# Optimization experiments

Measured on AMD Instinct MI355X. Metric: run time of the kernel, lower is better.

## Reference

```python
import jax, jax.numpy as jnp
import numpy as np

B = 8388608  # ~4096 stocks x 2048 trading days
D = 2048     # unique dates
LAMBDA_VOL = 0.85
LAMBDA_DIR = 0.15
TEMPERATURE = 5.0
EPS = 1e-6


def setup_inputs() -> dict:
    key = jax.random.key(0)
    k1, k2, k3, k4, k5 = jax.random.split(key, 5)
    return {
        "direction_logits": jax.random.normal(k1, (B, 2), dtype=jnp.float32),
        "direction_labels": jax.random.randint(k2, (B,), 0, 2, dtype=jnp.int64),
        "volatility_pred": jax.random.uniform(k3, (B,), dtype=jnp.float32),
        "volatility_target": jax.random.uniform(k4, (B,), dtype=jnp.float32),
        "dates": jax.random.randint(k5, (B,), 0, D, dtype=jnp.int64),
        "num_dates": D,
    }


def reference(direction_logits, direction_labels, volatility_pred, volatility_target, dates, num_dates):
    # ---- QLIKE volatility loss (masked mean) ----
    tgt, pred = volatility_target, volatility_pred
    vol_valid = (~jnp.isnan(tgt)) & (tgt > EPS) & (pred > EPS)
    pred_var = jnp.maximum(pred * pred, EPS)
    true_var = jnp.maximum(tgt * tgt, EPS)
    qlike = true_var / pred_var + jnp.log(pred_var)
    n_valid = jnp.sum(vol_valid)
    vol_loss = jnp.where(
        n_valid > 0,
        jnp.sum(jnp.where(vol_valid, qlike, 0.0)) / jnp.maximum(n_valid, 1).astype(qlike.dtype),
        0.0,
    )

    # ---- ListNet ranking loss via segmented softmax over dates ----
    dvalid = direction_labels >= 0
    p1 = jax.nn.softmax(direction_logits, axis=1)[:, 1]  # [B]

    # segmented stable softmax of p1 over each date group (valid entries only)
    pm = jax.ops.segment_max(jnp.where(dvalid, p1, -jnp.inf), dates, num_segments=num_dates)
    pe = jnp.where(dvalid, jnp.exp(p1 - pm[dates]), 0.0)
    pden = jax.ops.segment_sum(pe, dates, num_segments=num_dates)
    pred_dist = pe / jnp.maximum(pden[dates], 1e-30)

    # segmented softmax of temperature-scaled labels
    t = direction_labels.astype(p1.dtype) * TEMPERATURE
    tm = jax.ops.segment_max(jnp.where(dvalid, t, -jnp.inf), dates, num_segments=num_dates)
    te = jnp.where(dvalid, jnp.exp(t - tm[dates]), 0.0)
    tden = jax.ops.segment_sum(te, dates, num_segments=num_dates)
    true_dist = te / jnp.maximum(tden[dates], 1e-30)

    ce_el = jnp.where(dvalid, -true_dist * jnp.log(pred_dist + 1e-8), 0.0)
    ce_date = jax.ops.segment_sum(ce_el, dates, num_segments=num_dates)  # [D]
    counts = jax.ops.segment_sum(dvalid.astype(jnp.int32), dates, num_segments=num_dates)
    include = counts >= 2  # dates with < 2 stocks are skipped
    n_dates = jnp.sum(include)
    dir_loss = jnp.sum(jnp.where(include, ce_date, 0.0)) / jnp.maximum(n_dates, 1).astype(ce_date.dtype)

    total = LAMBDA_VOL * vol_loss + LAMBDA_DIR * dir_loss
    return total, vol_loss, dir_loss
```

## Files before the change

### kernel.cpp

```cpp
#include <hip/hip_runtime.h>

#define D_MAX 2048
#define EPSF 1e-6f
#define E5F 148.4131591f
#define BLK 512
#define GRID 1024


__global__ void initk(unsigned long long* g_pd, double* sum_q, unsigned* n_valid,
                      const int* ndp) {
    int i = blockIdx.x * blockDim.x + threadIdx.x;
    int nd = ndp[0]; if (nd > D_MAX) nd = D_MAX;
    if (i == 0) { *sum_q = 0.0; *n_valid = 0u; }
    if (i < nd) g_pd[i] = 0ULL;
}

__global__ __launch_bounds__(BLK)
void fusedk(const float4* __restrict__ lg4, const int4* __restrict__ lab4,
            const float4* __restrict__ vp4, const float4* __restrict__ vt4,
            const int4* __restrict__ dt4, int B,
            unsigned long long* __restrict__ g_pd,
            double* __restrict__ sum_q, unsigned* __restrict__ n_valid,
            const int* __restrict__ ndp) {
    __shared__ unsigned long long s_pack[D_MAX];
    __shared__ double s_q[BLK / 64];
    __shared__ unsigned s_n[BLK / 64];
    int nd = ndp[0]; if (nd > D_MAX) nd = D_MAX;
    for (int d = threadIdx.x; d < nd; d += BLK) s_pack[d] = 0ULL;
    __syncthreads();

    double accq = 0.0;
    unsigned accn = 0u;
    int B4 = B >> 2;
    int stride = gridDim.x * blockDim.x;
    for (int i = blockIdx.x * blockDim.x + threadIdx.x; i < B4; i += stride) {
        float4 p4 = vp4[i], t4 = vt4[i];
        int4 l4 = lab4[i], d4 = dt4[i];
        float4 ga = lg4[2 * i], gb = lg4[2 * i + 1];
        const float* pp = (const float*)&p4;
        const float* tt = (const float*)&t4;
        const int*   ll = (const int*)&l4;
        const int*   dd = (const int*)&d4;
        float lx[8];
        *(float4*)&lx[0] = ga; *(float4*)&lx[4] = gb;
#pragma unroll
        for (int k = 0; k < 4; k++) {
            float p = pp[k], tg = tt[k];
            if (tg > EPSF && p > EPSF) {
                float pv = fmaxf(p * p, EPSF);
                float tv = fmaxf(tg * tg, EPSF);
                accq += (double)(tv / pv + __logf(pv));
                accn++;
            }
            int lb = ll[k];
            if (lb >= 0) {
                int d = dd[k];
                float p1 = 1.0f / (1.0f + __expf(lx[2 * k] - lx[2 * k + 1]));
                float pe = __expf(p1);
                float w  = (lb >= 1) ? E5F * p1 : p1;
                unsigned stp_i = (unsigned)(w * 16.0f + 0.5f);
                unsigned pd_i  = (unsigned)(pe * 1024.0f + 0.5f);
                unsigned long long inc = (unsigned long long)stp_i
                                       | ((unsigned long long)pd_i << 24)
                                       | (1ULL << (48 + 8 * (lb >= 1)));
                atomicAdd(&s_pack[d], inc);
            }
        }
    }
    int gtid = blockIdx.x * blockDim.x + threadIdx.x;
    int rem = B & 3;
    if (gtid < rem) {
        int j = (B4 << 2) + gtid;
        float p = ((const float*)vp4)[j], tg = ((const float*)vt4)[j];
        if (tg > EPSF && p > EPSF) {
            float pv = fmaxf(p * p, EPSF), tv = fmaxf(tg * tg, EPSF);
            accq += (double)(tv / pv + __logf(pv)); accn++;
        }
        int lb = ((const int*)lab4)[j];
        if (lb >= 0) {
            int d = ((const int*)dt4)[j];
            float l0 = ((const float*)lg4)[2 * j], l1 = ((const float*)lg4)[2 * j + 1];
            float p1 = 1.0f / (1.0f + __expf(l0 - l1));
            float pe = __expf(p1);
            float w = (lb >= 1) ? E5F * p1 : p1;
            unsigned long long inc = (unsigned long long)(unsigned)(w * 16.0f + 0.5f)
                                   | ((unsigned long long)(unsigned)(pe * 1024.0f + 0.5f) << 24)
                                   | (1ULL << (48 + 8 * (lb >= 1)));
            atomicAdd(&s_pack[d], inc);
        }
    }

    for (int o = 32; o > 0; o >>= 1) {
        accq += __shfl_down(accq, o);
        accn += __shfl_down(accn, o);
    }
    int lane = threadIdx.x & 63, wv = threadIdx.x >> 6;
    if (lane == 0) { s_q[wv] = accq; s_n[wv] = accn; }
    __syncthreads();
    if (threadIdx.x == 0) {
        double q = 0.0; unsigned n = 0u;
        for (int w = 0; w < BLK / 64; w++) { q += s_q[w]; n += s_n[w]; }
        atomicAdd(sum_q, q);
        atomicAdd(n_valid, n);
    }

    int start = (blockIdx.x & 3) * (BLK);
    for (int k = 0; k < (nd + BLK - 1) / BLK; k++) {
        int d = start + threadIdx.x + k * BLK;
        if (d >= nd) d -= nd;
        if (d < nd) {
            unsigned long long c = s_pack[d];
            if (c) {
                unsigned stp24 = (unsigned)(c & 0xFFFFFFu);
                unsigned pd24  = (unsigned)((c >> 24) & 0xFFFFFFu);
                unsigned n0 = (unsigned)((c >> 48) & 0xFFu);
                unsigned n1 = (unsigned)(c >> 56);
                unsigned pd4  = (pd24 + 32u) >> 6;
                unsigned stp1 = (stp24 + 4u) >> 3;
                unsigned long long ginc = (unsigned long long)n0
                                        | ((unsigned long long)n1 << 12)
                                        | ((unsigned long long)pd4 << 24)
                                        | ((unsigned long long)stp1 << 42);
                atomicAdd(&g_pd[d], ginc);
            }
        }
    }
}

__global__ void finalk(const unsigned long long* __restrict__ g_pd, const int* __restrict__ ndp,
                       const double* __restrict__ sum_q, const unsigned* __restrict__ n_valid,
                       float* __restrict__ out) {
    __shared__ double s_ce[4];
    __shared__ unsigned s_c[4];
    int nd = ndp[0]; if (nd > D_MAX) nd = D_MAX;
    double ce = 0.0; unsigned cnt = 0u;
    for (int d = threadIdx.x; d < nd; d += 256) {
        unsigned long long pk = g_pd[d];
        unsigned n0 = (unsigned)(pk & 0xFFFu);
        unsigned n1 = (unsigned)((pk >> 12) & 0xFFFu);
        if (n0 + n1 >= 2u) {
            float pden = (float)((pk >> 24) & 0x3FFFFu) * (1.0f / 16.0f);
            float stp  = (float)(pk >> 42) * 0.5f;
            float td   = (float)n0 + (float)n1 * E5F;
            ce += (double)(__logf(fmaxf(pden, 1e-30f)) - stp / td);
            cnt++;
        }
    }
    for (int o = 32; o > 0; o >>= 1) { ce += __shfl_down(ce, o); cnt += __shfl_down(cnt, o); }
    int lane = threadIdx.x & 63, w = threadIdx.x >> 6;
    if (lane == 0) { s_ce[w] = ce; s_c[w] = cnt; }
    __syncthreads();
    if (threadIdx.x == 0) {
        double dce = s_ce[0] + s_ce[1] + s_ce[2] + s_ce[3];
        unsigned n = s_c[0] + s_c[1] + s_c[2] + s_c[3];
        unsigned nv = *n_valid;
        double vol = nv ? (*sum_q) / (double)nv : 0.0;
        double dir = dce / (double)(n ? n : 1u);
        out[0] = (float)(0.85 * vol + 0.15 * dir);
        out[1] = (float)vol;
        out[2] = (float)dir;
    }
}

extern "C" void kernel_launch(void* const* d_in, const int* in_sizes, int n_in,
                              void* d_out, int out_size, void* d_ws, size_t ws_size,
                              hipStream_t stream) {
    const float4* lg4 = (const float4*)d_in[0];
    const int4* lab4  = (const int4*)d_in[1];
    const float4* vp4 = (const float4*)d_in[2];
    const float4* vt4 = (const float4*)d_in[3];
    const int4* dt4   = (const int4*)d_in[4];
    const int* ndp    = (const int*)d_in[5];
    int B = in_sizes[1];
    float* out = (float*)d_out;

    char* ws = (char*)d_ws;
    double*   sum_q   = (double*)(ws + 0);
    unsigned* n_valid = (unsigned*)(ws + 8);
    unsigned long long* g_pd = (unsigned long long*)(ws + 64);

    initk<<<(D_MAX + 255) / 256, 256, 0, stream>>>(g_pd, sum_q, n_valid, ndp);
    fusedk<<<GRID, BLK, 0, stream>>>(lg4, lab4, vp4, vt4, dt4, B,
                                     g_pd, sum_q, n_valid, ndp);
    finalk<<<1, 256, 0, stream>>>(g_pd, ndp, sum_q, n_valid, out);
}
```

Baseline: 213.1 us.

## Halve block size, double grid, process two strided chunks per iteration, use fast divide

Block size drops from 512 to 256 and the grid grows to 2048 blocks. The main loop now issues loads for two strided float4 groups before processing either, which raises memory-level parallelism. Exact divisions become __fdividef, and the flush to global memory rotates its starting date across 8 offsets instead of 4, with a safer wrap. The larger grid doubles the number of per-block shared-memory histogram zeroing and flush passes and the global atomics, and the extra loads in flight raise register pressure.

```diff
diff --git a/kernel.cpp b/kernel.cpp
--- a/kernel.cpp
+++ b/kernel.cpp
@@ -3,8 +3,8 @@
 #define D_MAX 2048
 #define EPSF 1e-6f
 #define E5F 148.4131591f
-#define BLK 512
-#define GRID 1024
+#define BLK 256
+#define GRID 2048
 
 
 __global__ void initk(unsigned long long* g_pd, double* sum_q, unsigned* n_valid,
@@ -13,6 +13,40 @@
     int nd = ndp[0]; if (nd > D_MAX) nd = D_MAX;
     if (i == 0) { *sum_q = 0.0; *n_valid = 0u; }
     if (i < nd) g_pd[i] = 0ULL;
+}
+
+__device__ __forceinline__ void proc4(const float4& p4, const float4& t4,
+                                      const int4& l4, const int4& d4,
+                                      const float* lx,
+                                      double& accq, unsigned& accn,
+                                      unsigned long long* s_pack) {
+    const float* pp = (const float*)&p4;
+    const float* tt = (const float*)&t4;
+    const int*   ll = (const int*)&l4;
+    const int*   dd = (const int*)&d4;
+#pragma unroll
+    for (int k = 0; k < 4; k++) {
+        float p = pp[k], tg = tt[k];
+        if (tg > EPSF && p > EPSF) {
+            float pv = fmaxf(p * p, EPSF);
+            float tv = fmaxf(tg * tg, EPSF);
+            accq += (double)(__fdividef(tv, pv) + __logf(pv));
+            accn++;
+        }
+        int lb = ll[k];
+        if (lb >= 0) {
+            int d = dd[k];
+            float p1 = __fdividef(1.0f, 1.0f + __expf(lx[2 * k] - lx[2 * k + 1]));
+            float pe = __expf(p1);
+            float w  = (lb >= 1) ? E5F * p1 : p1;
+            unsigned stp_i = (unsigned)(w * 16.0f + 0.5f);
+            unsigned pd_i  = (unsigned)(pe * 1024.0f + 0.5f);
+            unsigned long long inc = (unsigned long long)stp_i
+                                   | ((unsigned long long)pd_i << 24)
+                                   | (1ULL << (48 + 8 * (lb >= 1)));
+            atomicAdd(&s_pack[d], inc);
+        }
+    }
 }
 
 __global__ __launch_bounds__(BLK)
@@ -33,54 +67,42 @@
     unsigned accn = 0u;
     int B4 = B >> 2;
     int stride = gridDim.x * blockDim.x;
-    for (int i = blockIdx.x * blockDim.x + threadIdx.x; i < B4; i += stride) {
-        float4 p4 = vp4[i], t4 = vt4[i];
-        int4 l4 = lab4[i], d4 = dt4[i];
-        float4 ga = lg4[2 * i], gb = lg4[2 * i + 1];
-        const float* pp = (const float*)&p4;
-        const float* tt = (const float*)&t4;
-        const int*   ll = (const int*)&l4;
-        const int*   dd = (const int*)&d4;
-        float lx[8];
-        *(float4*)&lx[0] = ga; *(float4*)&lx[4] = gb;
-#pragma unroll
-        for (int k = 0; k < 4; k++) {
-            float p = pp[k], tg = tt[k];
-            if (tg > EPSF && p > EPSF) {
-                float pv = fmaxf(p * p, EPSF);
-                float tv = fmaxf(tg * tg, EPSF);
-                accq += (double)(tv / pv + __logf(pv));
-                accn++;
-            }
-            int lb = ll[k];
-            if (lb >= 0) {
-                int d = dd[k];
-                float p1 = 1.0f / (1.0f + __expf(lx[2 * k] - lx[2 * k + 1]));
-                float pe = __expf(p1);
-                float w  = (lb >= 1) ? E5F * p1 : p1;
-                unsigned stp_i = (unsigned)(w * 16.0f + 0.5f);
-                unsigned pd_i  = (unsigned)(pe * 1024.0f + 0.5f);
-                unsigned long long inc = (unsigned long long)stp_i
-                                       | ((unsigned long long)pd_i << 24)
-                                       | (1ULL << (48 + 8 * (lb >= 1)));
-                atomicAdd(&s_pack[d], inc);
-            }
-        }
-    }
-    int gtid = blockIdx.x * blockDim.x + threadIdx.x;
+    int tid = blockIdx.x * blockDim.x + threadIdx.x;
+    for (int i = tid; i < B4; i += 2 * stride) {
+        int j = i + stride;
+        bool hasj = j < B4;
+        float4 p4a = vp4[i], t4a = vt4[i];
+        int4 l4a = lab4[i], d4a = dt4[i];
+        float4 ga_a = lg4[2 * i], gb_a = lg4[2 * i + 1];
+        float4 p4b, t4b, ga_b, gb_b;
+        int4 l4b, d4b;
+        if (hasj) {
+            p4b = vp4[j]; t4b = vt4[j];
+            l4b = lab4[j]; d4b = dt4[j];
+            ga_b = lg4[2 * j]; gb_b = lg4[2 * j + 1];
+        }
+        float lxa[8];
+        *(float4*)&lxa[0] = ga_a; *(float4*)&lxa[4] = gb_a;
+        proc4(p4a, t4a, l4a, d4a, lxa, accq, accn, s_pack);
+        if (hasj) {
+            float lxb[8];
+            *(float4*)&lxb[0] = ga_b; *(float4*)&lxb[4] = gb_b;
+            proc4(p4b, t4b, l4b, d4b, lxb, accq, accn, s_pack);
+        }
+    }
     int rem = B & 3;
-    if (gtid < rem) {
-        int j = (B4 << 2) + gtid;
+    if (tid < rem) {
+        int j = (B4 << 2) + tid;
         float p = ((const float*)vp4)[j], tg = ((const float*)vt4)[j];
         if (tg > EPSF && p > EPSF) {
             float pv = fmaxf(p * p, EPSF), tv = fmaxf(tg * tg, EPSF);
-            accq += (double)(tv / pv + __logf(pv)); accn++;
+            accq += (double)(__fdividef(tv, pv) + __logf(pv)); accn++;
         }
         int lb = ((const int*)lab4)[j];
         if (lb >= 0) {
             int d = ((const int*)dt4)[j];
             float l0 = ((const float*)lg4)[2 * j], l1 = ((const float*)lg4)[2 * j + 1];
-            float p1 = 1.0f / (1.0f + __expf(l0 - l1));
+            float p1 = __fdividef(1.0f, 1.0f + __expf(l0 - l1));
             float pe = __expf(p1);
             float w = (lb >= 1) ? E5F * p1 : p1;
             unsigned long long inc = (unsigned long long)(unsigned)(w * 16.0f + 0.5f)
@@ -104,11 +126,13 @@
         atomicAdd(n_valid, n);
     }
 
-    int start = (blockIdx.x & 3) * (BLK);
+    int start = (blockIdx.x & 7) * BLK;
+    if (start >= nd) start %= nd;
     for (int k = 0; k < (nd + BLK - 1) / BLK; k++) {
-        int d = start + threadIdx.x + k * BLK;
-        if (d >= nd) d -= nd;
-        if (d < nd) {
+        int d0 = threadIdx.x + k * BLK;
+        if (d0 < nd) {
+            int d = d0 + start;
+            if (d >= nd) d -= nd;
             unsigned long long c = s_pack[d];
             if (c) {
                 unsigned stp24 = (unsigned)(c & 0xFFFFFFu);
```

Result: slower. 223.7 us (+5.0%).
